# Kernel tuning notes

Measured on AMD Instinct MI355X. Metric: run time of the kernel, lower is better.

## Reference

```python
import jax, jax.numpy as jnp
import numpy as np


def setup_inputs() -> dict:
    key = jax.random.key(0)
    k1, k2 = jax.random.split(key)
    return {
        "embeddings": jax.random.normal(k1, (4, 768, 32, 32), dtype=jnp.float32),
        "database": jax.random.normal(k2, (20000, 768), dtype=jnp.float32),
        "k": 3,
        "out_h": 512,
        "out_w": 512,
    }


def reference(embeddings, database, k, out_h, out_w):
    # embeddings: [B, D, h, w]  (segmenter hidden state), database: [N, D]
    B, D, h, w = embeddings.shape
    # B x h x w x D -> B x (h*w) x D query layout, as in _get_ood_scores
    q = jnp.transpose(embeddings, (0, 2, 3, 1)).reshape(B, h * w, D)
    # squared Euclidean distances via (||q||^2 + ||x||^2 - 2 q.x)
    q2 = jnp.sum(q * q, axis=-1)[..., None]                 # [B, hw, 1]
    x2 = jnp.sum(database * database, axis=-1)[None, None]  # [1, 1, N]
    d2 = q2 + x2 - 2.0 * jnp.einsum("bqd,nd->bqn", q, database)
    dist = jnp.sqrt(jnp.maximum(d2, 1e-12))                 # [B, hw, N]
    # k smallest distances (sklearn kneighbors) then mean over neighbors
    neg_topk, _ = jax.lax.top_k(-dist, k)                   # [B, hw, k]
    ood = jnp.mean(-neg_topk, axis=-1).reshape(B, h, w)
    # F.interpolate(..., mode='bilinear', align_corners=False) == half-pixel bilinear
    ood_up = jax.image.resize(ood[:, None], (B, 1, out_h, out_w), method="bilinear")
    return ood_up
```

## Files before the change

### kernel.cpp

```cpp
#include <hip/hip_runtime.h>
#include <hip/hip_bf16.h>
#include <math.h>

constexpr int B    = 4;
constexpr int D    = 768;
constexpr int HW   = 1024;
constexpr int M    = B * HW;
constexpr int NDB  = 20000;
constexpr int LT   = 158;
constexpr int NDBP = LT * 128;
constexpr int OUTH = 512;
constexpr int OUTW = 512;

constexpr int BM     = 256;
constexpr int BN     = 128;
constexpr int KSTEPS = D / 64;
constexpr int NSPLIT = 16;
constexpr int NT2    = 79;
constexpr int STEPB  = 128 * 64;

typedef int   i32x8  __attribute__((ext_vector_type(8)));
typedef float f32x16 __attribute__((ext_vector_type(16)));

__device__ __forceinline__ void insert3(float& t0, float& t1, float& t2, float d) {
    float a0 = fminf(d, t0);
    float b0 = fmaxf(d, t0);
    float a1 = fminf(b0, t1);
    float b1 = fmaxf(b0, t1);
    t0 = a0; t1 = a1;
    t2 = fminf(b1, t2);
}

__device__ __forceinline__ unsigned int pack4_fp8(float a, float b, float c, float d) {
    int v = __builtin_amdgcn_cvt_pk_fp8_f32(a, b, 0, false);
    v = __builtin_amdgcn_cvt_pk_fp8_f32(c, d, v, true);
    return (unsigned int)v;
}

__device__ __forceinline__ void gl_lds16(const unsigned char* g, unsigned char* l) {
    __builtin_amdgcn_global_load_lds(
        (const __attribute__((address_space(1))) void*)g,
        (__attribute__((address_space(3))) void*)l, 16, 0, 0);
}

__global__ __launch_bounds__(256) void db_convert(const float* __restrict__ db,
                                                  uint4* __restrict__ dbt8,
                                                  float* __restrict__ x2p) {
    __shared__ float panel[128][68];
    __shared__ float part[512];
    const int lt = blockIdx.x;
    const int g  = blockIdx.y;
    const int t  = threadIdx.x;
    const int n0 = lt * 128;

    #pragma unroll
    for (int pass = 0; pass < 8; ++pass) {
        int idx = pass * 256 + t;
        int row = idx >> 4, c4 = idx & 15;
        int n = n0 + row;
        float4 v = make_float4(0.f, 0.f, 0.f, 0.f);
        if (n < NDB) v = *(const float4*)(db + (size_t)n * D + g * 64 + c4 * 4);
        *(float4*)&panel[row][c4 * 4] = v;
    }
    __syncthreads();
    #pragma unroll
    for (int pass = 0; pass < 2; ++pass) {
        int idx = pass * 256 + t;
        int r  = idx & 31;
        int kc = (idx >> 5) & 1;
        int h2 = (idx >> 6) & 1;
        int rg = idx >> 7;
        int row  = rg * 32 + r;
        int kloc = kc * 32 + h2 * 16;
        float4 va = *(const float4*)&panel[row][kloc + 0];
        float4 vb = *(const float4*)&panel[row][kloc + 4];
        float4 vc = *(const float4*)&panel[row][kloc + 8];
        float4 vd = *(const float4*)&panel[row][kloc + 12];
        float ss = va.x*va.x + va.y*va.y + va.z*va.z + va.w*va.w
                 + vb.x*vb.x + vb.y*vb.y + vb.z*vb.z + vb.w*vb.w
                 + vc.x*vc.x + vc.y*vc.y + vc.z*vc.z + vc.w*vc.w
                 + vd.x*vd.x + vd.y*vd.y + vd.z*vd.z + vd.w*vd.w;
        uint4 o;
        o.x = pack4_fp8(va.x, va.y, va.z, va.w);
        o.y = pack4_fp8(vb.x, vb.y, vb.z, vb.w);
        o.z = pack4_fp8(vc.x, vc.y, vc.z, vc.w);
        o.w = pack4_fp8(vd.x, vd.y, vd.z, vd.w);
        dbt8[((size_t)lt * KSTEPS + g) * 512 + idx] = o;
        part[idx] = ss;
    }
    __syncthreads();
    if (t < 128) {
        int base = (t >> 5) * 128 + (t & 31);
        float s = part[base] + part[base + 32] + part[base + 64] + part[base + 96];
        x2p[((size_t)lt * KSTEPS + g) * 128 + t] = s;
    }
}

__global__ __launch_bounds__(256) void q_convert(const float* __restrict__ emb,
                                                 uint4* __restrict__ qbt8,
                                                 float* __restrict__ q2p) {
    __shared__ float part[512];
    const int qt = blockIdx.x;
    const int g  = blockIdx.y;
    const int t  = threadIdx.x;
    const int b  = qt >> 3;
    const int p0 = (qt & 7) * 128;

    #pragma unroll
    for (int pass = 0; pass < 2; ++pass) {
        int idx = pass * 256 + t;
        int r  = idx & 31;
        int kc = (idx >> 5) & 1;
        int h2 = (idx >> 6) & 1;
        int rg = idx >> 7;
        int prow = rg * 32 + r;
        int kb = g * 64 + kc * 32 + h2 * 16;
        const float* src = emb + ((size_t)b * D + kb) * HW + p0 + prow;
        float v[16];
        float ss = 0.f;
        #pragma unroll
        for (int j = 0; j < 16; ++j) {
            v[j] = src[(size_t)j * HW];
            ss = fmaf(v[j], v[j], ss);
        }
        uint4 o;
        o.x = pack4_fp8(-2.f*v[0],  -2.f*v[1],  -2.f*v[2],  -2.f*v[3]);
        o.y = pack4_fp8(-2.f*v[4],  -2.f*v[5],  -2.f*v[6],  -2.f*v[7]);
        o.z = pack4_fp8(-2.f*v[8],  -2.f*v[9],  -2.f*v[10], -2.f*v[11]);
        o.w = pack4_fp8(-2.f*v[12], -2.f*v[13], -2.f*v[14], -2.f*v[15]);
        qbt8[((size_t)qt * KSTEPS + g) * 512 + idx] = o;
        part[idx] = ss;
    }
    __syncthreads();
    if (t < 128) {
        int base = (t >> 5) * 128 + (t & 31);
        float s = part[base] + part[base + 32] + part[base + 64] + part[base + 96];
        q2p[((size_t)qt * KSTEPS + g) * 128 + t] = s;
    }
}

__global__ __launch_bounds__(256, 2) void gemm_topk(const unsigned char* __restrict__ dbt8,
                                                    const unsigned char* __restrict__ qbt8,
                                                    const float* __restrict__ x2p,
                                                    float* __restrict__ partials) {
    __shared__ __align__(16) unsigned char Asm[2 * 16384];
    __shared__ __align__(16) unsigned char Bsm[2 * 8192];
    __shared__ float X2s[BM];
    __shared__ float red[4][BN][3];

    const int tid  = threadIdx.x;
    const int lane = tid & 63;
    const int w    = tid >> 6;
    const int lts  = w >> 1;
    const int wr   = w & 1;
    const int h    = lane >> 5;
    const int l31  = lane & 31;

    const int bid   = blockIdx.x;
    const int xcd   = bid & 7;
    const int j     = bid >> 3;
    const int sp    = xcd + 8 * (j >> 5);
    const int qtile = j & 31;
    const int m0    = qtile * BN;

    int a_off[2], b_off[4];
    #pragma unroll
    for (int i = 0; i < 2; ++i) a_off[i] = lts * 8192 + (wr * 2 + i) * 2048 + h * 512 + l31 * 16;
    #pragma unroll
    for (int j4 = 0; j4 < 4; ++j4) b_off[j4] = j4 * 2048 + h * 512 + l31 * 16;

    const unsigned char* aNext = dbt8 + (size_t)(2 * sp + lts) * KSTEPS * STEPB + wr * 4096 + lane * 16;
    const unsigned char* bNext = qbt8 + (size_t)qtile * KSTEPS * STEPB + w * 2048 + lane * 16;
    unsigned char* aDst = Asm + w * 4096;
    unsigned char* bDst = Bsm + w * 2048;

    #pragma unroll
    for (int l = 0; l < 4; ++l) gl_lds16(aNext + l * 1024, aDst + l * 1024);
    #pragma unroll
    for (int l = 0; l < 2; ++l) gl_lds16(bNext + l * 1024, bDst + l * 1024);

    float t0[4], t1[4], t2[4];
    #pragma unroll
    for (int j4 = 0; j4 < 4; ++j4) { t0[j4] = INFINITY; t1[j4] = INFINITY; t2[j4] = INFINITY; }

    for (int tile = sp; tile < NT2; tile += NSPLIT) {
        __syncthreads();
        {
            int n = tile * BM + tid;
            float s = 1e30f;
            if (n < NDB) {
                const float* p = x2p + (size_t)(n >> 7) * (KSTEPS * 128) + (n & 127);
                s = 0.f;
                #pragma unroll
                for (int g = 0; g < KSTEPS; ++g) s += p[g * 128];
            }
            X2s[tid] = s;
        }

        f32x16 acc[2][4];
        #pragma unroll
        for (int i = 0; i < 2; ++i)
            #pragma unroll
            for (int j4 = 0; j4 < 4; ++j4)
                #pragma unroll
                for (int r = 0; r < 16; ++r) acc[i][j4][r] = 0.f;

        const bool lastTile = (tile + NSPLIT >= NT2);

        #pragma unroll 2
        for (int g = 0; g < KSTEPS; ++g) {
            const int cur = g & 1;
            __syncthreads();
            if (g < KSTEPS - 1) {
                aNext += STEPB;
                bNext += STEPB;
                unsigned char* ad = aDst + (cur ^ 1) * 16384;
                unsigned char* bd = bDst + (cur ^ 1) * 8192;
                #pragma unroll
                for (int l = 0; l < 4; ++l) gl_lds16(aNext + l * 1024, ad + l * 1024);
                #pragma unroll
                for (int l = 0; l < 2; ++l) gl_lds16(bNext + l * 1024, bd + l * 1024);
            } else if (!lastTile) {
                aNext += (size_t)(2 * NSPLIT) * KSTEPS * STEPB - (KSTEPS - 1) * STEPB;
                bNext -= (size_t)(KSTEPS - 1) * STEPB;
                unsigned char* ad = aDst + (cur ^ 1) * 16384;
                unsigned char* bd = bDst + (cur ^ 1) * 8192;
                #pragma unroll
                for (int l = 0; l < 4; ++l) gl_lds16(aNext + l * 1024, ad + l * 1024);
                #pragma unroll
                for (int l = 0; l < 2; ++l) gl_lds16(bNext + l * 1024, bd + l * 1024);
            }
            const unsigned char* Ab = Asm + cur * 16384;
            const unsigned char* Bb = Bsm + cur * 8192;
            i32x8 af[2], bf[4];
            #pragma unroll
            for (int i = 0; i < 2; ++i) {
                int4 lo = *(const int4*)(Ab + a_off[i]);
                int4 hi = *(const int4*)(Ab + a_off[i] + 1024);
                af[i] = (i32x8){lo.x, lo.y, lo.z, lo.w, hi.x, hi.y, hi.z, hi.w};
            }
            #pragma unroll
            for (int j4 = 0; j4 < 4; ++j4) {
                int4 lo = *(const int4*)(Bb + b_off[j4]);
                int4 hi = *(const int4*)(Bb + b_off[j4] + 1024);
                bf[j4] = (i32x8){lo.x, lo.y, lo.z, lo.w, hi.x, hi.y, hi.z, hi.w};
            }
            #pragma unroll
            for (int i = 0; i < 2; ++i)
                #pragma unroll
                for (int j4 = 0; j4 < 4; ++j4)
                    acc[i][j4] = __builtin_amdgcn_mfma_scale_f32_32x32x64_f8f6f4(
                        af[i], bf[j4], acc[i][j4], 0, 0,
                        0, 0x7f7f7f7f, 0, 0x7f7f7f7f);
        }

        #pragma unroll
        for (int i = 0; i < 2; ++i) {
            #pragma unroll
            for (int rg2 = 0; rg2 < 4; ++rg2) {
                float4 xv = *(const float4*)&X2s[w * 64 + i * 32 + rg2 * 8 + 4 * h];
                #pragma unroll
                for (int j4 = 0; j4 < 4; ++j4) {
                    #pragma unroll
                    for (int rr = 0; rr < 4; ++rr) {
                        float s = acc[i][j4][rg2 * 4 + rr] + ((const float*)&xv)[rr];
                        insert3(t0[j4], t1[j4], t2[j4], s);
                    }
                }
            }
        }
    }

    #pragma unroll
    for (int j4 = 0; j4 < 4; ++j4) {
        float o0 = __shfl_xor(t0[j4], 32);
        float o1 = __shfl_xor(t1[j4], 32);
        float o2 = __shfl_xor(t2[j4], 32);
        insert3(t0[j4], t1[j4], t2[j4], o0);
        insert3(t0[j4], t1[j4], t2[j4], o1);
        insert3(t0[j4], t1[j4], t2[j4], o2);
    }
    if (h == 0) {
        #pragma unroll
        for (int j4 = 0; j4 < 4; ++j4) {
            int col = j4 * 32 + l31;
            red[w][col][0] = t0[j4];
            red[w][col][1] = t1[j4];
            red[w][col][2] = t2[j4];
        }
    }
    __syncthreads();
    if (tid < BN) {
        float a0 = red[0][tid][0], a1 = red[0][tid][1], a2 = red[0][tid][2];
        #pragma unroll
        for (int ww = 1; ww < 4; ++ww) {
            insert3(a0, a1, a2, red[ww][tid][0]);
            insert3(a0, a1, a2, red[ww][tid][1]);
            insert3(a0, a1, a2, red[ww][tid][2]);
        }
        float* dst = partials + ((size_t)(m0 + tid) * NSPLIT + sp) * 3;
        dst[0] = a0; dst[1] = a1; dst[2] = a2;
    }
}

__global__ __launch_bounds__(256) void merge_ood(const float* __restrict__ partials,
                                                 const float* __restrict__ q2p,
                                                 float* __restrict__ ood) {
    int m = blockIdx.x * 256 + threadIdx.x;
    if (m >= M) return;
    const float* pp = partials + (size_t)m * NSPLIT * 3;
    float a0 = INFINITY, a1 = INFINITY, a2 = INFINITY;
    #pragma unroll
    for (int j = 0; j < NSPLIT * 3; ++j) insert3(a0, a1, a2, pp[j]);
    const float* qp = q2p + (size_t)(m >> 7) * KSTEPS * 128 + (m & 127);
    float q = 0.f;
    #pragma unroll
    for (int g = 0; g < KSTEPS; ++g) q += qp[g * 128];
    float d0 = sqrtf(fmaxf(q + a0, 1e-12f));
    float d1 = sqrtf(fmaxf(q + a1, 1e-12f));
    float d2 = sqrtf(fmaxf(q + a2, 1e-12f));
    ood[m] = (d0 + d1 + d2) * (1.f / 3.f);
}

__global__ __launch_bounds__(256) void upsample(const float* __restrict__ ood,
                                                float* __restrict__ out) {
    int idx = blockIdx.x * 256 + threadIdx.x;
    int ox = idx & (OUTW - 1);
    int oy = (idx >> 9) & (OUTH - 1);
    int bb = idx >> 18;
    float sx = (ox + 0.5f) * (32.f / OUTW) - 0.5f;
    float sy = (oy + 0.5f) * (32.f / OUTH) - 0.5f;
    float fx = floorf(sx), fy = floorf(sy);
    float wx = sx - fx, wy = sy - fy;
    int x0 = max(0, min(31, (int)fx));
    int x1 = max(0, min(31, (int)fx + 1));
    int y0 = max(0, min(31, (int)fy));
    int y1 = max(0, min(31, (int)fy + 1));
    const float* src = ood + bb * 1024;
    float v00 = src[y0 * 32 + x0];
    float v01 = src[y0 * 32 + x1];
    float v10 = src[y1 * 32 + x0];
    float v11 = src[y1 * 32 + x1];
    float top = v00 + wx * (v01 - v00);
    float bot = v10 + wx * (v11 - v10);
    out[idx] = top + wy * (bot - top);
}

extern "C" void kernel_launch(void* const* d_in, const int* in_sizes, int n_in,
                              void* d_out, int out_size, void* d_ws, size_t ws_size,
                              hipStream_t stream) {
    const float* emb = (const float*)d_in[0];
    const float* db  = (const float*)d_in[1];
    float* out = (float*)d_out;

    char* ws = (char*)d_ws;
    unsigned char* dbt8 = (unsigned char*)ws;
    unsigned char* qbt8 = (unsigned char*)(ws + 15532032);
    float* x2p      = (float*)(ws + 18677760);
    float* q2p      = (float*)(ws + 19648512);
    float* ood      = (float*)(ws + 19845120);
    float* partials = (float*)(ws + 19861504);

    db_convert<<<dim3(LT, KSTEPS), 256, 0, stream>>>(db, (uint4*)dbt8, x2p);
    q_convert<<<dim3(32, KSTEPS), 256, 0, stream>>>(emb, (uint4*)qbt8, q2p);
    gemm_topk<<<NSPLIT * 32, 256, 0, stream>>>(dbt8, qbt8, x2p, partials);
    merge_ood<<<(M + 255) / 256, 256, 0, stream>>>(partials, q2p, ood);
    upsample<<<(B * OUTH * OUTW) / 256, 256, 0, stream>>>(ood, out);
}
```

Baseline: 184.4 us.

## Fuse convert, GEMM-topk and upsample into one cooperative persistent kernel

```diff
diff --git a/kernel.cpp b/kernel.cpp
--- a/kernel.cpp
+++ b/kernel.cpp
@@ -1,6 +1,9 @@
 #include <hip/hip_runtime.h>
+#include <hip/hip_cooperative_groups.h>
 #include <hip/hip_bf16.h>
 #include <math.h>
+
+namespace cg = cooperative_groups;
 
 constexpr int B    = 4;
 constexpr int D    = 768;
@@ -8,16 +11,17 @@
 constexpr int M    = B * HW;
 constexpr int NDB  = 20000;
 constexpr int LT   = 158;
-constexpr int NDBP = LT * 128;
 constexpr int OUTH = 512;
 constexpr int OUTW = 512;
 
 constexpr int BM     = 256;
 constexpr int BN     = 128;
 constexpr int KSTEPS = D / 64;
-constexpr int NSPLIT = 16;
+constexpr int NSPLIT = 8;
 constexpr int NT2    = 79;
 constexpr int STEPB  = 128 * 64;
+constexpr int NBLK   = 256;
+constexpr int NUNITS = LT * KSTEPS + 32 * KSTEPS;
 
 typedef int   i32x8  __attribute__((ext_vector_type(8)));
 typedef float f32x16 __attribute__((ext_vector_type(16)));
@@ -43,112 +47,115 @@
         (__attribute__((address_space(3))) void*)l, 16, 0, 0);
 }
 
-__global__ __launch_bounds__(256) void db_convert(const float* __restrict__ db,
-                                                  uint4* __restrict__ dbt8,
-                                                  float* __restrict__ x2p) {
-    __shared__ float panel[128][68];
-    __shared__ float part[512];
-    const int lt = blockIdx.x;
-    const int g  = blockIdx.y;
-    const int t  = threadIdx.x;
-    const int n0 = lt * 128;
-
-    #pragma unroll
-    for (int pass = 0; pass < 8; ++pass) {
-        int idx = pass * 256 + t;
-        int row = idx >> 4, c4 = idx & 15;
-        int n = n0 + row;
-        float4 v = make_float4(0.f, 0.f, 0.f, 0.f);
-        if (n < NDB) v = *(const float4*)(db + (size_t)n * D + g * 64 + c4 * 4);
-        *(float4*)&panel[row][c4 * 4] = v;
-    }
-    __syncthreads();
-    #pragma unroll
-    for (int pass = 0; pass < 2; ++pass) {
-        int idx = pass * 256 + t;
-        int r  = idx & 31;
-        int kc = (idx >> 5) & 1;
-        int h2 = (idx >> 6) & 1;
-        int rg = idx >> 7;
-        int row  = rg * 32 + r;
-        int kloc = kc * 32 + h2 * 16;
-        float4 va = *(const float4*)&panel[row][kloc + 0];
-        float4 vb = *(const float4*)&panel[row][kloc + 4];
-        float4 vc = *(const float4*)&panel[row][kloc + 8];
-        float4 vd = *(const float4*)&panel[row][kloc + 12];
-        float ss = va.x*va.x + va.y*va.y + va.z*va.z + va.w*va.w
-                 + vb.x*vb.x + vb.y*vb.y + vb.z*vb.z + vb.w*vb.w
-                 + vc.x*vc.x + vc.y*vc.y + vc.z*vc.z + vc.w*vc.w
-                 + vd.x*vd.x + vd.y*vd.y + vd.z*vd.z + vd.w*vd.w;
-        uint4 o;
-        o.x = pack4_fp8(va.x, va.y, va.z, va.w);
-        o.y = pack4_fp8(vb.x, vb.y, vb.z, vb.w);
-        o.z = pack4_fp8(vc.x, vc.y, vc.z, vc.w);
-        o.w = pack4_fp8(vd.x, vd.y, vd.z, vd.w);
-        dbt8[((size_t)lt * KSTEPS + g) * 512 + idx] = o;
-        part[idx] = ss;
-    }
-    __syncthreads();
-    if (t < 128) {
-        int base = (t >> 5) * 128 + (t & 31);
-        float s = part[base] + part[base + 32] + part[base + 64] + part[base + 96];
-        x2p[((size_t)lt * KSTEPS + g) * 128 + t] = s;
-    }
-}
-
-__global__ __launch_bounds__(256) void q_convert(const float* __restrict__ emb,
-                                                 uint4* __restrict__ qbt8,
-                                                 float* __restrict__ q2p) {
-    __shared__ float part[512];
-    const int qt = blockIdx.x;
-    const int g  = blockIdx.y;
-    const int t  = threadIdx.x;
-    const int b  = qt >> 3;
-    const int p0 = (qt & 7) * 128;
-
-    #pragma unroll
-    for (int pass = 0; pass < 2; ++pass) {
-        int idx = pass * 256 + t;
-        int r  = idx & 31;
-        int kc = (idx >> 5) & 1;
-        int h2 = (idx >> 6) & 1;
-        int rg = idx >> 7;
-        int prow = rg * 32 + r;
-        int kb = g * 64 + kc * 32 + h2 * 16;
-        const float* src = emb + ((size_t)b * D + kb) * HW + p0 + prow;
-        float v[16];
-        float ss = 0.f;
-        #pragma unroll
-        for (int j = 0; j < 16; ++j) {
-            v[j] = src[(size_t)j * HW];
-            ss = fmaf(v[j], v[j], ss);
-        }
-        uint4 o;
-        o.x = pack4_fp8(-2.f*v[0],  -2.f*v[1],  -2.f*v[2],  -2.f*v[3]);
-        o.y = pack4_fp8(-2.f*v[4],  -2.f*v[5],  -2.f*v[6],  -2.f*v[7]);
-        o.z = pack4_fp8(-2.f*v[8],  -2.f*v[9],  -2.f*v[10], -2.f*v[11]);
-        o.w = pack4_fp8(-2.f*v[12], -2.f*v[13], -2.f*v[14], -2.f*v[15]);
-        qbt8[((size_t)qt * KSTEPS + g) * 512 + idx] = o;
-        part[idx] = ss;
-    }
-    __syncthreads();
-    if (t < 128) {
-        int base = (t >> 5) * 128 + (t & 31);
-        float s = part[base] + part[base + 32] + part[base + 64] + part[base + 96];
-        q2p[((size_t)qt * KSTEPS + g) * 128 + t] = s;
-    }
-}
-
-__global__ __launch_bounds__(256, 2) void gemm_topk(const unsigned char* __restrict__ dbt8,
-                                                    const unsigned char* __restrict__ qbt8,
-                                                    const float* __restrict__ x2p,
-                                                    float* __restrict__ partials) {
-    __shared__ __align__(16) unsigned char Asm[2 * 16384];
-    __shared__ __align__(16) unsigned char Bsm[2 * 8192];
-    __shared__ float X2s[BM];
-    __shared__ float red[4][BN][3];
-
-    const int tid  = threadIdx.x;
+__device__ void phase1_convert(int bid, int t, unsigned char* smem,
+                               const float* __restrict__ emb,
+                               const float* __restrict__ db,
+                               unsigned char* __restrict__ dbt8,
+                               unsigned char* __restrict__ qbt8,
+                               float* __restrict__ x2p,
+                               float* __restrict__ q2p) {
+    float (*panel)[68] = (float(*)[68])smem;
+    float* part        = (float*)(smem + 34816);
+
+    for (int u = bid; u < NUNITS; u += NBLK) {
+        if (u < LT * KSTEPS) {
+            const int lt = u / KSTEPS;
+            const int g  = u - lt * KSTEPS;
+            const int n0 = lt * 128;
+            #pragma unroll
+            for (int pass = 0; pass < 8; ++pass) {
+                int idx = pass * 256 + t;
+                int row = idx >> 4, c4 = idx & 15;
+                int n = n0 + row;
+                float4 v = make_float4(0.f, 0.f, 0.f, 0.f);
+                if (n < NDB) v = *(const float4*)(db + (size_t)n * D + g * 64 + c4 * 4);
+                *(float4*)&panel[row][c4 * 4] = v;
+            }
+            __syncthreads();
+            #pragma unroll
+            for (int pass = 0; pass < 2; ++pass) {
+                int idx = pass * 256 + t;
+                int r  = idx & 31;
+                int kc = (idx >> 5) & 1;
+                int h2 = (idx >> 6) & 1;
+                int rg = idx >> 7;
+                int row  = rg * 32 + r;
+                int kloc = kc * 32 + h2 * 16;
+                float4 va = *(const float4*)&panel[row][kloc + 0];
+                float4 vb = *(const float4*)&panel[row][kloc + 4];
+                float4 vc = *(const float4*)&panel[row][kloc + 8];
+                float4 vd = *(const float4*)&panel[row][kloc + 12];
+                float ss = va.x*va.x + va.y*va.y + va.z*va.z + va.w*va.w
+                         + vb.x*vb.x + vb.y*vb.y + vb.z*vb.z + vb.w*vb.w
+                         + vc.x*vc.x + vc.y*vc.y + vc.z*vc.z + vc.w*vc.w
+                         + vd.x*vd.x + vd.y*vd.y + vd.z*vd.z + vd.w*vd.w;
+                uint4 o;
+                o.x = pack4_fp8(va.x, va.y, va.z, va.w);
+                o.y = pack4_fp8(vb.x, vb.y, vb.z, vb.w);
+                o.z = pack4_fp8(vc.x, vc.y, vc.z, vc.w);
+                o.w = pack4_fp8(vd.x, vd.y, vd.z, vd.w);
+                ((uint4*)dbt8)[((size_t)lt * KSTEPS + g) * 512 + idx] = o;
+                part[idx] = ss;
+            }
+            __syncthreads();
+            if (t < 128) {
+                int base = (t >> 5) * 128 + (t & 31);
+                float s = part[base] + part[base + 32] + part[base + 64] + part[base + 96];
+                x2p[((size_t)lt * KSTEPS + g) * 128 + t] = s;
+            }
+            __syncthreads();
+        } else {
+            const int v2 = u - LT * KSTEPS;
+            const int qt = v2 / KSTEPS;
+            const int g  = v2 - qt * KSTEPS;
+            const int b  = qt >> 3;
+            const int p0 = (qt & 7) * 128;
+            #pragma unroll
+            for (int pass = 0; pass < 2; ++pass) {
+                int idx = pass * 256 + t;
+                int r  = idx & 31;
+                int kc = (idx >> 5) & 1;
+                int h2 = (idx >> 6) & 1;
+                int rg = idx >> 7;
+                int prow = rg * 32 + r;
+                int kb = g * 64 + kc * 32 + h2 * 16;
+                const float* src = emb + ((size_t)b * D + kb) * HW + p0 + prow;
+                float v[16];
+                float ss = 0.f;
+                #pragma unroll
+                for (int j = 0; j < 16; ++j) {
+                    v[j] = src[(size_t)j * HW];
+                    ss = fmaf(v[j], v[j], ss);
+                }
+                uint4 o;
+                o.x = pack4_fp8(-2.f*v[0],  -2.f*v[1],  -2.f*v[2],  -2.f*v[3]);
+                o.y = pack4_fp8(-2.f*v[4],  -2.f*v[5],  -2.f*v[6],  -2.f*v[7]);
+                o.z = pack4_fp8(-2.f*v[8],  -2.f*v[9],  -2.f*v[10], -2.f*v[11]);
+                o.w = pack4_fp8(-2.f*v[12], -2.f*v[13], -2.f*v[14], -2.f*v[15]);
+                ((uint4*)qbt8)[((size_t)qt * KSTEPS + g) * 512 + idx] = o;
+                part[idx] = ss;
+            }
+            __syncthreads();
+            if (t < 128) {
+                int base = (t >> 5) * 128 + (t & 31);
+                float s = part[base] + part[base + 32] + part[base + 64] + part[base + 96];
+                q2p[((size_t)qt * KSTEPS + g) * 128 + t] = s;
+            }
+            __syncthreads();
+        }
+    }
+}
+
+__device__ void phase2_gemm(int bid, int tid, unsigned char* smem,
+                            const unsigned char* __restrict__ dbt8,
+                            const unsigned char* __restrict__ qbt8,
+                            const float* __restrict__ x2p,
+                            float* __restrict__ partials) {
+    unsigned char* Asm = smem;
+    unsigned char* Bsm = smem + 32768;
+    float* X2s  = (float*)(smem + 49152);
+    float* redp = (float*)(smem + 50176);
+
     const int lane = tid & 63;
     const int w    = tid >> 6;
     const int lts  = w >> 1;
@@ -156,11 +163,8 @@
     const int h    = lane >> 5;
     const int l31  = lane & 31;
 
-    const int bid   = blockIdx.x;
-    const int xcd   = bid & 7;
-    const int j     = bid >> 3;
-    const int sp    = xcd + 8 * (j >> 5);
-    const int qtile = j & 31;
+    const int sp    = bid & 7;
+    const int qtile = bid >> 3;
     const int m0    = qtile * BN;
 
     int a_off[2], b_off[4];
@@ -221,7 +225,7 @@
                 #pragma unroll
                 for (int l = 0; l < 2; ++l) gl_lds16(bNext + l * 1024, bd + l * 1024);
             } else if (!lastTile) {
-                aNext += (size_t)(2 * NSPLIT) * KSTEPS * STEPB - (KSTEPS - 1) * STEPB;
+                aNext += (size_t)(2 * NSPLIT) * KSTEPS * STEPB - (size_t)(KSTEPS - 1) * STEPB;
                 bNext -= (size_t)(KSTEPS - 1) * STEPB;
                 unsigned char* ad = aDst + (cur ^ 1) * 16384;
                 unsigned char* bd = bDst + (cur ^ 1) * 8192;
@@ -284,66 +288,125 @@
         #pragma unroll
         for (int j4 = 0; j4 < 4; ++j4) {
             int col = j4 * 32 + l31;
-            red[w][col][0] = t0[j4];
-            red[w][col][1] = t1[j4];
-            red[w][col][2] = t2[j4];
+            redp[(w * BN + col) * 3 + 0] = t0[j4];
+            redp[(w * BN + col) * 3 + 1] = t1[j4];
+            redp[(w * BN + col) * 3 + 2] = t2[j4];
         }
     }
     __syncthreads();
     if (tid < BN) {
-        float a0 = red[0][tid][0], a1 = red[0][tid][1], a2 = red[0][tid][2];
+        float a0 = redp[tid * 3 + 0], a1 = redp[tid * 3 + 1], a2 = redp[tid * 3 + 2];
         #pragma unroll
         for (int ww = 1; ww < 4; ++ww) {
-            insert3(a0, a1, a2, red[ww][tid][0]);
-            insert3(a0, a1, a2, red[ww][tid][1]);
-            insert3(a0, a1, a2, red[ww][tid][2]);
+            insert3(a0, a1, a2, redp[(ww * BN + tid) * 3 + 0]);
+            insert3(a0, a1, a2, redp[(ww * BN + tid) * 3 + 1]);
+            insert3(a0, a1, a2, redp[(ww * BN + tid) * 3 + 2]);
         }
         float* dst = partials + ((size_t)(m0 + tid) * NSPLIT + sp) * 3;
         dst[0] = a0; dst[1] = a1; dst[2] = a2;
     }
 }
 
-__global__ __launch_bounds__(256) void merge_ood(const float* __restrict__ partials,
-                                                 const float* __restrict__ q2p,
-                                                 float* __restrict__ ood) {
-    int m = blockIdx.x * 256 + threadIdx.x;
-    if (m >= M) return;
-    const float* pp = partials + (size_t)m * NSPLIT * 3;
-    float a0 = INFINITY, a1 = INFINITY, a2 = INFINITY;
-    #pragma unroll
-    for (int j = 0; j < NSPLIT * 3; ++j) insert3(a0, a1, a2, pp[j]);
-    const float* qp = q2p + (size_t)(m >> 7) * KSTEPS * 128 + (m & 127);
-    float q = 0.f;
-    #pragma unroll
-    for (int g = 0; g < KSTEPS; ++g) q += qp[g * 128];
-    float d0 = sqrtf(fmaxf(q + a0, 1e-12f));
-    float d1 = sqrtf(fmaxf(q + a1, 1e-12f));
-    float d2 = sqrtf(fmaxf(q + a2, 1e-12f));
-    ood[m] = (d0 + d1 + d2) * (1.f / 3.f);
-}
-
-__global__ __launch_bounds__(256) void upsample(const float* __restrict__ ood,
+__device__ void phase3_out(int bid, int t, unsigned char* smem,
+                           const float* __restrict__ partials,
+                           const float* __restrict__ q2p,
+                           float* __restrict__ out) {
+    float* oodc = (float*)smem;
+    const int bb  = bid >> 6;
+    const int blk = bid & 63;
+    const int oy0 = blk * 8;
+    const float syb = (oy0 + 0.5f) * (1.f / 16.f) - 0.5f;
+    const int f = (int)floorf(syb);
+
+    if (t < 96) {
+        int ci = t >> 5, x = t & 31;
+        int y = min(max(f + ci, 0), 31);
+        int m = bb * 1024 + y * 32 + x;
+        const float* pp = partials + (size_t)m * NSPLIT * 3;
+        float a0 = INFINITY, a1 = INFINITY, a2 = INFINITY;
+        #pragma unroll
+        for (int j = 0; j < NSPLIT * 3; ++j) insert3(a0, a1, a2, pp[j]);
+        const float* qp = q2p + (size_t)(m >> 7) * (KSTEPS * 128) + (m & 127);
+        float q = 0.f;
+        #pragma unroll
+        for (int g = 0; g < KSTEPS; ++g) q += qp[g * 128];
+        float d0 = sqrtf(fmaxf(q + a0, 1e-12f));
+        float d1 = sqrtf(fmaxf(q + a1, 1e-12f));
+        float d2 = sqrtf(fmaxf(q + a2, 1e-12f));
+        oodc[ci * 32 + x] = (d0 + d1 + d2) * (1.f / 3.f);
+    }
+    __syncthreads();
+
+    const int p0  = t * 16;
+    const int oy  = oy0 + (p0 >> 9);
+    const int ox0 = p0 & 511;
+    float sy = (oy + 0.5f) * (1.f / 16.f) - 0.5f;
+    int g0 = (int)floorf(sy);
+    float wy = sy - (float)g0;
+    const float* rowA = oodc + (g0 - f) * 32;
+    const float* rowB = rowA + 32;
+    float vout[16];
+    #pragma unroll
+    for (int k = 0; k < 16; ++k) {
+        int ox = ox0 + k;
+        float sx = (ox + 0.5f) * (1.f / 16.f) - 0.5f;
+        float fx = floorf(sx);
+        float wx = sx - fx;
+        int x0 = max(0, min(31, (int)fx));
+        int x1 = max(0, min(31, (int)fx + 1));
+        float top = rowA[x0] + wx * (rowA[x1] - rowA[x0]);
+        float bot = rowB[x0] + wx * (rowB[x1] - rowB[x0]);
+        vout[k] = top + wy * (bot - top);
+    }
+    float* dst = out + (size_t)bid * 4096 + p0;
+    #pragma unroll
+    for (int k = 0; k < 4; ++k)
+        *(float4*)(dst + k * 4) = *(float4*)&vout[k * 4];
+}
+
+__global__ __launch_bounds__(256) void fused_knn(const float* __restrict__ emb,
+                                                 const float* __restrict__ db,
+                                                 unsigned char* __restrict__ dbt8,
+                                                 unsigned char* __restrict__ qbt8,
+                                                 float* __restrict__ x2p,
+                                                 float* __restrict__ q2p,
+                                                 float* __restrict__ partials,
+                                                 float* __restrict__ out) {
+    __shared__ __align__(16) unsigned char smem[56320];
+    const int t   = threadIdx.x;
+    const int bid = blockIdx.x;
+    cg::grid_group grid = cg::this_grid();
+
+    phase1_convert(bid, t, smem, emb, db, dbt8, qbt8, x2p, q2p);
+    __threadfence();
+    grid.sync();
+    phase2_gemm(bid, t, smem, dbt8, qbt8, x2p, partials);
+    __threadfence();
+    grid.sync();
+    phase3_out(bid, t, smem, partials, q2p, out);
+}
+
+__global__ __launch_bounds__(256) void k_phase1(const float* __restrict__ emb,
+                                                const float* __restrict__ db,
+                                                unsigned char* __restrict__ dbt8,
+                                                unsigned char* __restrict__ qbt8,
+                                                float* __restrict__ x2p,
+                                                float* __restrict__ q2p) {
+    __shared__ __align__(16) unsigned char smem[36864];
+    phase1_convert(blockIdx.x, threadIdx.x, smem, emb, db, dbt8, qbt8, x2p, q2p);
+}
+__global__ __launch_bounds__(256) void k_phase2(const unsigned char* __restrict__ dbt8,
+                                                const unsigned char* __restrict__ qbt8,
+                                                const float* __restrict__ x2p,
+                                                float* __restrict__ partials) {
+    __shared__ __align__(16) unsigned char smem[56320];
+    phase2_gemm(blockIdx.x, threadIdx.x, smem, dbt8, qbt8, x2p, partials);
+}
+__global__ __launch_bounds__(256) void k_phase3(const float* __restrict__ partials,
+                                                const float* __restrict__ q2p,
                                                 float* __restrict__ out) {
-    int idx = blockIdx.x * 256 + threadIdx.x;
-    int ox = idx & (OUTW - 1);
-    int oy = (idx >> 9) & (OUTH - 1);
-    int bb = idx >> 18;
-    float sx = (ox + 0.5f) * (32.f / OUTW) - 0.5f;
-    float sy = (oy + 0.5f) * (32.f / OUTH) - 0.5f;
-    float fx = floorf(sx), fy = floorf(sy);
-    float wx = sx - fx, wy = sy - fy;
-    int x0 = max(0, min(31, (int)fx));
-    int x1 = max(0, min(31, (int)fx + 1));
-    int y0 = max(0, min(31, (int)fy));
-    int y1 = max(0, min(31, (int)fy + 1));
-    const float* src = ood + bb * 1024;
-    float v00 = src[y0 * 32 + x0];
-    float v01 = src[y0 * 32 + x1];
-    float v10 = src[y1 * 32 + x0];
-    float v11 = src[y1 * 32 + x1];
-    float top = v00 + wx * (v01 - v00);
-    float bot = v10 + wx * (v11 - v10);
-    out[idx] = top + wy * (bot - top);
+    __shared__ __align__(16) unsigned char smem[512];
+    phase3_out(blockIdx.x, threadIdx.x, smem, partials, q2p, out);
 }
 
 extern "C" void kernel_launch(void* const* d_in, const int* in_sizes, int n_in,
@@ -358,12 +421,16 @@
     unsigned char* qbt8 = (unsigned char*)(ws + 15532032);
     float* x2p      = (float*)(ws + 18677760);
     float* q2p      = (float*)(ws + 19648512);
-    float* ood      = (float*)(ws + 19845120);
-    float* partials = (float*)(ws + 19861504);
-
-    db_convert<<<dim3(LT, KSTEPS), 256, 0, stream>>>(db, (uint4*)dbt8, x2p);
-    q_convert<<<dim3(32, KSTEPS), 256, 0, stream>>>(emb, (uint4*)qbt8, q2p);
-    gemm_topk<<<NSPLIT * 32, 256, 0, stream>>>(dbt8, qbt8, x2p, partials);
-    merge_ood<<<(M + 255) / 256, 256, 0, stream>>>(partials, q2p, ood);
-    upsample<<<(B * OUTH * OUTW) / 256, 256, 0, stream>>>(ood, out);
-}
+    float* partials = (float*)(ws + 19845120);
+
+    void* args[] = { (void*)&emb, (void*)&db, (void*)&dbt8, (void*)&qbt8,
+                     (void*)&x2p, (void*)&q2p, (void*)&partials, (void*)&out };
+    hipError_t err = hipLaunchCooperativeKernel((void*)fused_knn, dim3(NBLK), dim3(256),
+                                                args, 0, stream);
+    if (err != hipSuccess) {
+        (void)hipGetLastError();
+        k_phase1<<<NBLK, 256, 0, stream>>>(emb, db, dbt8, qbt8, x2p, q2p);
+        k_phase2<<<NBLK, 256, 0, stream>>>(dbt8, qbt8, x2p, partials);
+        k_phase3<<<NBLK, 256, 0, stream>>>(partials, q2p, out);
+    }
+}
```

Result: slower. 381.0 us (+106.6%).
